# Kernel optimization log

Hardware: AMD Instinct MI355X
Metric: run time of the kernel (lower is better)

## Reference

```python
import jax, jax.numpy as jnp
import numpy as np

HIDDEN = 128
INPUT_DIM = 1
NUM_CLASSES = 2


def setup_inputs() -> dict:
    key = jax.random.key(0)
    ks = jax.random.split(key, 7)
    B, T = 256, 1024
    s_ih = 1.0 / np.sqrt(HIDDEN)
    x = jax.random.normal(ks[0], (B, T, INPUT_DIM), dtype=jnp.float32)
    W_ih = jax.random.uniform(ks[1], (HIDDEN, INPUT_DIM), jnp.float32, -s_ih, s_ih)
    W_hh = jax.random.uniform(ks[2], (HIDDEN, HIDDEN), jnp.float32, -s_ih, s_ih)
    b_ih = jax.random.uniform(ks[3], (HIDDEN,), jnp.float32, -s_ih, s_ih)
    b_hh = jax.random.uniform(ks[4], (HIDDEN,), jnp.float32, -s_ih, s_ih)
    W_fc = jax.random.uniform(ks[5], (NUM_CLASSES, HIDDEN), jnp.float32, -s_ih, s_ih)
    b_fc = jax.random.uniform(ks[6], (NUM_CLASSES,), jnp.float32, -s_ih, s_ih)
    return {"x": x, "W_ih": W_ih, "W_hh": W_hh, "b_ih": b_ih,
            "b_hh": b_hh, "W_fc": W_fc, "b_fc": b_fc}


def reference(x, W_ih, W_hh, b_ih, b_hh, W_fc, b_fc):
    B = x.shape[0]
    # Precompute input projection for all timesteps: [B,T,H]
    xp = jnp.einsum('bti,hi->bth', x, W_ih) + b_ih + b_hh
    h0 = jnp.zeros((B, HIDDEN), dtype=x.dtype)

    def step(h, xp_t):
        h_new = jnp.tanh(xp_t + h @ W_hh.T)  # [B,H]
        return h_new, h_new

    _, hs = jax.lax.scan(step, h0, jnp.swapaxes(xp, 0, 1))  # hs: [T,B,H]
    out = jnp.swapaxes(hs, 0, 1)  # [B,T,H]
    logits = jnp.einsum('bth,ch->btc', out, W_fc) + b_fc  # [B,T,C]
    return logits
```

## Files before the change

kernel.cpp:

```cpp
#include <hip/hip_runtime.h>

typedef float f32x2 __attribute__((ext_vector_type(2)));
typedef float f32x4 __attribute__((ext_vector_type(4)));

#define BB 256
#define TT 1024
#define HH 128
#define CC 2

__device__ __forceinline__ float ftanh(float u) {
    float e = __expf(2.0f * u);
    float r = __builtin_amdgcn_rcpf(e + 1.0f);
    return fmaf(-2.0f, r, 1.0f);
}

__device__ __forceinline__ float bcast(float v, int j) {
    return __int_as_float(__builtin_amdgcn_readlane(__float_as_int(v), j));
}

#define DPP_ADD(v, ctrl)                                                     \
    ((v) + __int_as_float(__builtin_amdgcn_mov_dpp(                          \
         __float_as_int(v), (ctrl), 0xF, 0xF, true)))

__device__ __forceinline__ float wave_sum(float q) {
    q = DPP_ADD(q, 0xB1);
    q = DPP_ADD(q, 0x4E);
    q = DPP_ADD(q, 0x124);
    q = DPP_ADD(q, 0x128);
    return bcast(q, 0) + bcast(q, 16) + bcast(q, 32) + bcast(q, 48);
}

__global__ __launch_bounds__(256, 1) void rnn_kernel(
    const float* __restrict__ x, const float* __restrict__ W_ih,
    const float* __restrict__ W_hh, const float* __restrict__ b_ih,
    const float* __restrict__ b_hh, const float* __restrict__ W_fc,
    const float* __restrict__ b_fc, float* __restrict__ out)
{
    const int b   = blockIdx.x;
    const int tid = threadIdx.x;
    const int l   = tid & 63;
    const int wv  = tid >> 6;
    const int lq  = l & 31;
    const int kb  = wv << 5;
    const int rA  = l, rB = l + 64;
    const int rF  = kb + lq;

    __shared__ float xs[TT + 8];
    __shared__ f32x2 p2[2][4][64];
    __shared__ f32x2 qp[4][4];

    {
        const f32x4* xr = (const f32x4*)(x + (size_t)b * TT);
        ((f32x4*)xs)[tid] = xr[tid];
    }
    if (tid < 8) xs[TT + tid] = 0.f;

    const float wih  = W_ih[rF];
    const float bias = b_ih[rF] + b_hh[rF];
    const float wf0  = 0.5f * W_fc[rF];
    const float wf1  = 0.5f * W_fc[HH + rF];
    const float bf0  = b_fc[0], bf1 = b_fc[1];

    float wa[32], wb[32];
    {
        const f32x4* a4 = (const f32x4*)(W_hh + (size_t)rA * HH + kb);
        const f32x4* b4 = (const f32x4*)(W_hh + (size_t)rB * HH + kb);
        #pragma unroll
        for (int j = 0; j < 8; ++j) {
            f32x4 va = a4[j], vb = b4[j];
            wa[4*j+0] = va.x; wa[4*j+1] = va.y; wa[4*j+2] = va.z; wa[4*j+3] = va.w;
            wb[4*j+0] = vb.x; wb[4*j+1] = vb.y; wb[4*j+2] = vb.z; wb[4*j+3] = vb.w;
        }
        #pragma unroll
        for (int k = 0; k < 32; ++k)
            asm volatile("" : "+v"(wa[k]), "+v"(wb[k]));
    }

    float hn = 0.f;
    float* o = out + (size_t)b * TT * CC;

    __syncthreads();
    float xcur = xs[0];

    #pragma unroll 4
    for (int t = 0; t < TT; ++t) {
        const int buf = t & 1, qb = t & 3;

        float aA0 = 0.f, aA1 = 0.f, aB0 = 0.f, aB1 = 0.f;
        #pragma unroll
        for (int k = 0; k < 32; k += 2) {
            float s0 = bcast(hn, k);
            float s1 = bcast(hn, k + 1);
            aA0 = fmaf(wa[k],     s0, aA0);
            aB0 = fmaf(wb[k],     s0, aB0);
            aA1 = fmaf(wa[k + 1], s1, aA1);
            aB1 = fmaf(wb[k + 1], s1, aB1);
        }
        f32x2 pr = { aA0 + aA1, aB0 + aB1 };
        p2[buf][wv][l] = pr;

        float q0 = wave_sum(wf0 * hn);
        float q1 = wave_sum(wf1 * hn);
        if (l == 0) qp[qb][wv] = f32x2{q0, q1};

        const float base  = fmaf(xcur, wih, bias);
        const float xnext = xs[t + 1];

        __syncthreads();

        if (t > 0 && tid == 0) {
            f32x2 s = (qp[qb][0] + qp[qb][1]) + (qp[qb][2] + qp[qb][3]);
            s.x += bf0; s.y += bf1;
            *(f32x2*)(o + (t - 1) * CC) = s;
        }

        const float* pf = (const float*)&p2[buf][0][0]
                        + ((((wv & 1) << 5) + lq) << 1) + (wv >> 1);
        float p0 = pf[0], p1 = pf[128], pv2 = pf[256], pv3 = pf[384];
        hn = ftanh(base + ((p0 + p1) + (pv2 + pv3)));
        xcur = xnext;
    }

    {
        float q0 = wave_sum(wf0 * hn);
        float q1 = wave_sum(wf1 * hn);
        if (l == 0) qp[0][wv] = f32x2{q0, q1};
    }
    __syncthreads();
    if (tid == 0) {
        f32x2 s = (qp[0][0] + qp[0][1]) + (qp[0][2] + qp[0][3]);
        s.x += bf0; s.y += bf1;
        *(f32x2*)(o + (TT - 1) * CC) = s;
    }
}

extern "C" void kernel_launch(void* const* d_in, const int* in_sizes, int n_in,
                              void* d_out, int out_size, void* d_ws, size_t ws_size,
                              hipStream_t stream) {
    const float* x    = (const float*)d_in[0];
    const float* W_ih = (const float*)d_in[1];
    const float* W_hh = (const float*)d_in[2];
    const float* b_ih = (const float*)d_in[3];
    const float* b_hh = (const float*)d_in[4];
    const float* W_fc = (const float*)d_in[5];
    const float* b_fc = (const float*)d_in[6];
    float* out = (float*)d_out;

    rnn_kernel<<<BB, 256, 0, stream>>>(x, W_ih, W_hh, b_ih, b_hh, W_fc, b_fc, out);
}
```

Measured before the change: 464.2 us.

## Process two batch rows per block with packed f32x2 FMAs

Each workgroup now advances two independent batch sequences at once, and the grid shrinks to half as many blocks. Weights are repacked as f32x2 pairs so the matvec can use packed FMA. The partial-sum LDS layout changes so each thread reads one f32x4 per row. The goal is to amortise the per-step barrier and latency over two recurrences and raise ILP, at the cost of only 128 blocks on a GPU with 256 CUs, which leaves many CUs idle.

Result: slower. 648.2 us (+39.6%).

```diff
diff --git a/kernel.cpp b/kernel.cpp
--- a/kernel.cpp
+++ b/kernel.cpp
@@ -7,6 +7,7 @@
 #define TT 1024
 #define HH 128
 #define CC 2
+#define NR 2
 
 __device__ __forceinline__ float ftanh(float u) {
     float e = __expf(2.0f * u);
@@ -45,15 +46,16 @@
     const int rA  = l, rB = l + 64;
     const int rF  = kb + lq;
 
-    __shared__ float xs[TT + 8];
-    __shared__ f32x2 p2[2][4][64];
-    __shared__ f32x2 qp[4][4];
+    __shared__ float xs[NR][TT + 8];
+    __shared__ float p2[2][NR][HH][4];
+    __shared__ f32x2 qp[4][NR][4];
 
-    {
-        const f32x4* xr = (const f32x4*)(x + (size_t)b * TT);
-        ((f32x4*)xs)[tid] = xr[tid];
+    #pragma unroll
+    for (int r = 0; r < NR; ++r) {
+        const f32x4* xr = (const f32x4*)(x + (size_t)(NR * b + r) * TT);
+        ((f32x4*)xs[r])[tid] = xr[tid];
     }
-    if (tid < 8) xs[TT + tid] = 0.f;
+    if (tid < 8) { xs[0][TT + tid] = 0.f; xs[1][TT + tid] = 0.f; }
 
     const float wih  = W_ih[rF];
     const float bias = b_ih[rF] + b_hh[rF];
@@ -61,76 +63,95 @@
     const float wf1  = 0.5f * W_fc[HH + rF];
     const float bf0  = b_fc[0], bf1 = b_fc[1];
 
-    float wa[32], wb[32];
+    f32x2 wr[32];
     {
         const f32x4* a4 = (const f32x4*)(W_hh + (size_t)rA * HH + kb);
         const f32x4* b4 = (const f32x4*)(W_hh + (size_t)rB * HH + kb);
         #pragma unroll
         for (int j = 0; j < 8; ++j) {
             f32x4 va = a4[j], vb = b4[j];
-            wa[4*j+0] = va.x; wa[4*j+1] = va.y; wa[4*j+2] = va.z; wa[4*j+3] = va.w;
-            wb[4*j+0] = vb.x; wb[4*j+1] = vb.y; wb[4*j+2] = vb.z; wb[4*j+3] = vb.w;
+            wr[4*j+0] = f32x2{va.x, vb.x};
+            wr[4*j+1] = f32x2{va.y, vb.y};
+            wr[4*j+2] = f32x2{va.z, vb.z};
+            wr[4*j+3] = f32x2{va.w, vb.w};
         }
-        #pragma unroll
-        for (int k = 0; k < 32; ++k)
-            asm volatile("" : "+v"(wa[k]), "+v"(wb[k]));
     }
 
-    float hn = 0.f;
-    float* o = out + (size_t)b * TT * CC;
+    float hn0 = 0.f, hn1 = 0.f;
+    float* oo = out + (size_t)(NR * b + (tid & 1)) * TT * CC;
 
     __syncthreads();
-    float xcur = xs[0];
+    float xc0 = xs[0][0], xc1 = xs[1][0];
 
     #pragma unroll 4
     for (int t = 0; t < TT; ++t) {
         const int buf = t & 1, qb = t & 3;
 
-        float aA0 = 0.f, aA1 = 0.f, aB0 = 0.f, aB1 = 0.f;
+        asm volatile("" : "+v"(wr[0]), "+v"(wr[1]), "+v"(wr[2]), "+v"(wr[3]),
+                          "+v"(wr[4]), "+v"(wr[5]), "+v"(wr[6]), "+v"(wr[7]));
+        asm volatile("" : "+v"(wr[8]), "+v"(wr[9]), "+v"(wr[10]), "+v"(wr[11]),
+                          "+v"(wr[12]), "+v"(wr[13]), "+v"(wr[14]), "+v"(wr[15]));
+        asm volatile("" : "+v"(wr[16]), "+v"(wr[17]), "+v"(wr[18]), "+v"(wr[19]),
+                          "+v"(wr[20]), "+v"(wr[21]), "+v"(wr[22]), "+v"(wr[23]));
+        asm volatile("" : "+v"(wr[24]), "+v"(wr[25]), "+v"(wr[26]), "+v"(wr[27]),
+                          "+v"(wr[28]), "+v"(wr[29]), "+v"(wr[30]), "+v"(wr[31]));
+
+        f32x2 a00 = {0.f,0.f}, a01 = {0.f,0.f};
+        f32x2 a10 = {0.f,0.f}, a11 = {0.f,0.f};
         #pragma unroll
         for (int k = 0; k < 32; k += 2) {
-            float s0 = bcast(hn, k);
-            float s1 = bcast(hn, k + 1);
-            aA0 = fmaf(wa[k],     s0, aA0);
-            aB0 = fmaf(wb[k],     s0, aB0);
-            aA1 = fmaf(wa[k + 1], s1, aA1);
-            aB1 = fmaf(wb[k + 1], s1, aB1);
+            float s00 = bcast(hn0, k), s01 = bcast(hn0, k + 1);
+            float s10 = bcast(hn1, k), s11 = bcast(hn1, k + 1);
+            a00 = __builtin_elementwise_fma(wr[k],     f32x2{s00, s00}, a00);
+            a10 = __builtin_elementwise_fma(wr[k],     f32x2{s10, s10}, a10);
+            a01 = __builtin_elementwise_fma(wr[k + 1], f32x2{s01, s01}, a01);
+            a11 = __builtin_elementwise_fma(wr[k + 1], f32x2{s11, s11}, a11);
         }
-        f32x2 pr = { aA0 + aA1, aB0 + aB1 };
-        p2[buf][wv][l] = pr;
+        f32x2 pr0 = a00 + a01, pr1 = a10 + a11;
 
-        float q0 = wave_sum(wf0 * hn);
-        float q1 = wave_sum(wf1 * hn);
-        if (l == 0) qp[qb][wv] = f32x2{q0, q1};
+        p2[buf][0][rA][wv] = pr0.x;  p2[buf][0][rB][wv] = pr0.y;
+        p2[buf][1][rA][wv] = pr1.x;  p2[buf][1][rB][wv] = pr1.y;
 
-        const float base  = fmaf(xcur, wih, bias);
-        const float xnext = xs[t + 1];
+        float q00 = wave_sum(wf0 * hn0), q01 = wave_sum(wf1 * hn0);
+        float q10 = wave_sum(wf0 * hn1), q11 = wave_sum(wf1 * hn1);
+        if (l == 0) {
+            qp[qb][0][wv] = f32x2{q00, q01};
+            qp[qb][1][wv] = f32x2{q10, q11};
+        }
+
+        const float base0 = fmaf(xc0, wih, bias);
+        const float base1 = fmaf(xc1, wih, bias);
+        xc0 = xs[0][t + 1];  xc1 = xs[1][t + 1];
 
         __syncthreads();
 
-        if (t > 0 && tid == 0) {
-            f32x2 s = (qp[qb][0] + qp[qb][1]) + (qp[qb][2] + qp[qb][3]);
+        if (t > 0 && tid < NR) {
+            f32x2 s = (qp[qb][tid][0] + qp[qb][tid][1])
+                    + (qp[qb][tid][2] + qp[qb][tid][3]);
             s.x += bf0; s.y += bf1;
-            *(f32x2*)(o + (t - 1) * CC) = s;
+            *(f32x2*)(oo + (t - 1) * CC) = s;
         }
 
-        const float* pf = (const float*)&p2[buf][0][0]
-                        + ((((wv & 1) << 5) + lq) << 1) + (wv >> 1);
-        float p0 = pf[0], p1 = pf[128], pv2 = pf[256], pv3 = pf[384];
-        hn = ftanh(base + ((p0 + p1) + (pv2 + pv3)));
-        xcur = xnext;
+        f32x4 c0 = *(const f32x4*)&p2[buf][0][rF][0];
+        f32x4 c1 = *(const f32x4*)&p2[buf][1][rF][0];
+        hn0 = ftanh(base0 + ((c0.x + c0.y) + (c0.z + c0.w)));
+        hn1 = ftanh(base1 + ((c1.x + c1.y) + (c1.z + c1.w)));
     }
 
     {
-        float q0 = wave_sum(wf0 * hn);
-        float q1 = wave_sum(wf1 * hn);
-        if (l == 0) qp[0][wv] = f32x2{q0, q1};
+        float q00 = wave_sum(wf0 * hn0), q01 = wave_sum(wf1 * hn0);
+        float q10 = wave_sum(wf0 * hn1), q11 = wave_sum(wf1 * hn1);
+        if (l == 0) {
+            qp[0][0][wv] = f32x2{q00, q01};
+            qp[0][1][wv] = f32x2{q10, q11};
+        }
     }
     __syncthreads();
-    if (tid == 0) {
-        f32x2 s = (qp[0][0] + qp[0][1]) + (qp[0][2] + qp[0][3]);
+    if (tid < NR) {
+        f32x2 s = (qp[0][tid][0] + qp[0][tid][1])
+                + (qp[0][tid][2] + qp[0][tid][3]);
         s.x += bf0; s.y += bf1;
-        *(f32x2*)(o + (TT - 1) * CC) = s;
+        *(f32x2*)(oo + (TT - 1) * CC) = s;
     }
 }
 
@@ -146,5 +167,5 @@
     const float* b_fc = (const float*)d_in[6];
     float* out = (float*)d_out;
 
-    rnn_kernel<<<BB, 256, 0, stream>>>(x, W_ih, W_hh, b_ih, b_hh, W_fc, b_fc, out);
+    rnn_kernel<<<BB / NR, 256, 0, stream>>>(x, W_ih, W_hh, b_ih, b_hh, W_fc, b_fc, out);
 }
```

## Pack two batch sequences per block and merge the FC lane reductions

Applied to the files above, without the earlier changes.

Each 512-thread block now runs two independent batch sequences, one per 256-thread group, so half as many blocks are launched and two recurrences share one CU and one barrier. The two output-class reductions are folded into one DPP reduction: the lower half-wave weights by class 0 and the upper half by class 1, which removes the 0.5 scaling and one full wave_sum per step. The empty asm register pin on the W_hh weights is dropped and launch bounds change to (512,2). The aim is to hide per-step latency by interleaving two recurrences on each SIMD. The risk is that the shared barrier couples the two groups and each CU now does twice the per-step work.

Measured after the change: 540.6 us. 16.5% more time.

```diff
diff --git a/kernel.cpp b/kernel.cpp
--- a/kernel.cpp
+++ b/kernel.cpp
@@ -7,6 +7,7 @@
 #define TT 1024
 #define HH 128
 #define CC 2
+#define NG 2
 
 __device__ __forceinline__ float ftanh(float u) {
     float e = __expf(2.0f * u);
@@ -22,15 +23,7 @@
     ((v) + __int_as_float(__builtin_amdgcn_mov_dpp(                          \
          __float_as_int(v), (ctrl), 0xF, 0xF, true)))
 
-__device__ __forceinline__ float wave_sum(float q) {
-    q = DPP_ADD(q, 0xB1);
-    q = DPP_ADD(q, 0x4E);
-    q = DPP_ADD(q, 0x124);
-    q = DPP_ADD(q, 0x128);
-    return bcast(q, 0) + bcast(q, 16) + bcast(q, 32) + bcast(q, 48);
-}
-
-__global__ __launch_bounds__(256, 1) void rnn_kernel(
+__global__ __launch_bounds__(512, 2) void rnn_kernel(
     const float* __restrict__ x, const float* __restrict__ W_ih,
     const float* __restrict__ W_hh, const float* __restrict__ b_ih,
     const float* __restrict__ b_hh, const float* __restrict__ W_fc,
@@ -38,27 +31,28 @@
 {
     const int b   = blockIdx.x;
     const int tid = threadIdx.x;
+    const int g   = tid >> 8;
+    const int t2  = tid & 255;
     const int l   = tid & 63;
-    const int wv  = tid >> 6;
+    const int wv  = (tid >> 6) & 3;
     const int lq  = l & 31;
     const int kb  = wv << 5;
     const int rA  = l, rB = l + 64;
     const int rF  = kb + lq;
 
-    __shared__ float xs[TT + 8];
-    __shared__ f32x2 p2[2][4][64];
-    __shared__ f32x2 qp[4][4];
+    __shared__ float xs[NG][TT + 8];
+    __shared__ f32x2 p2[2][NG][4][64];
+    __shared__ f32x2 qp[4][NG][4];
 
     {
-        const f32x4* xr = (const f32x4*)(x + (size_t)b * TT);
-        ((f32x4*)xs)[tid] = xr[tid];
+        const f32x4* xr = (const f32x4*)(x + (size_t)(NG * b + g) * TT);
+        ((f32x4*)xs[g])[t2] = xr[t2];
     }
-    if (tid < 8) xs[TT + tid] = 0.f;
+    if (t2 < 8) xs[g][TT + t2] = 0.f;
 
     const float wih  = W_ih[rF];
     const float bias = b_ih[rF] + b_hh[rF];
-    const float wf0  = 0.5f * W_fc[rF];
-    const float wf1  = 0.5f * W_fc[HH + rF];
+    const float wfs  = (l < 32) ? W_fc[rF] : W_fc[HH + rF];
     const float bf0  = b_fc[0], bf1 = b_fc[1];
 
     float wa[32], wb[32];
@@ -71,16 +65,13 @@
             wa[4*j+0] = va.x; wa[4*j+1] = va.y; wa[4*j+2] = va.z; wa[4*j+3] = va.w;
             wb[4*j+0] = vb.x; wb[4*j+1] = vb.y; wb[4*j+2] = vb.z; wb[4*j+3] = vb.w;
         }
-        #pragma unroll
-        for (int k = 0; k < 32; ++k)
-            asm volatile("" : "+v"(wa[k]), "+v"(wb[k]));
     }
 
     float hn = 0.f;
-    float* o = out + (size_t)b * TT * CC;
+    float* o = out + (size_t)(NG * b + g) * TT * CC;
 
     __syncthreads();
-    float xcur = xs[0];
+    float xcur = xs[g][0];
 
     #pragma unroll 4
     for (int t = 0; t < TT; ++t) {
@@ -97,24 +88,31 @@
             aB1 = fmaf(wb[k + 1], s1, aB1);
         }
         f32x2 pr = { aA0 + aA1, aB0 + aB1 };
-        p2[buf][wv][l] = pr;
+        p2[buf][g][wv][l] = pr;
 
-        float q0 = wave_sum(wf0 * hn);
-        float q1 = wave_sum(wf1 * hn);
-        if (l == 0) qp[qb][wv] = f32x2{q0, q1};
+        {
+            float q = wfs * hn;
+            q = DPP_ADD(q, 0xB1);
+            q = DPP_ADD(q, 0x4E);
+            q = DPP_ADD(q, 0x124);
+            q = DPP_ADD(q, 0x128);
+            float q0 = bcast(q, 0)  + bcast(q, 16);
+            float q1 = bcast(q, 32) + bcast(q, 48);
+            if (l == 0) qp[qb][g][wv] = f32x2{q0, q1};
+        }
 
         const float base  = fmaf(xcur, wih, bias);
-        const float xnext = xs[t + 1];
+        const float xnext = xs[g][t + 1];
 
         __syncthreads();
 
-        if (t > 0 && tid == 0) {
-            f32x2 s = (qp[qb][0] + qp[qb][1]) + (qp[qb][2] + qp[qb][3]);
+        if (t > 0 && t2 == 0) {
+            f32x2 s = (qp[qb][g][0] + qp[qb][g][1]) + (qp[qb][g][2] + qp[qb][g][3]);
             s.x += bf0; s.y += bf1;
             *(f32x2*)(o + (t - 1) * CC) = s;
         }
 
-        const float* pf = (const float*)&p2[buf][0][0]
+        const float* pf = (const float*)&p2[buf][g][0][0]
                         + ((((wv & 1) << 5) + lq) << 1) + (wv >> 1);
         float p0 = pf[0], p1 = pf[128], pv2 = pf[256], pv3 = pf[384];
         hn = ftanh(base + ((p0 + p1) + (pv2 + pv3)));
@@ -122,13 +120,18 @@
     }
 
     {
-        float q0 = wave_sum(wf0 * hn);
-        float q1 = wave_sum(wf1 * hn);
-        if (l == 0) qp[0][wv] = f32x2{q0, q1};
+        float q = wfs * hn;
+        q = DPP_ADD(q, 0xB1);
+        q = DPP_ADD(q, 0x4E);
+        q = DPP_ADD(q, 0x124);
+        q = DPP_ADD(q, 0x128);
+        float q0 = bcast(q, 0)  + bcast(q, 16);
+        float q1 = bcast(q, 32) + bcast(q, 48);
+        if (l == 0) qp[0][g][wv] = f32x2{q0, q1};
     }
     __syncthreads();
-    if (tid == 0) {
-        f32x2 s = (qp[0][0] + qp[0][1]) + (qp[0][2] + qp[0][3]);
+    if (t2 == 0) {
+        f32x2 s = (qp[0][g][0] + qp[0][g][1]) + (qp[0][g][2] + qp[0][g][3]);
         s.x += bf0; s.y += bf1;
         *(f32x2*)(o + (TT - 1) * CC) = s;
     }
@@ -146,5 +149,5 @@
     const float* b_fc = (const float*)d_in[6];
     float* out = (float*)d_out;
 
-    rnn_kernel<<<BB, 256, 0, stream>>>(x, W_ih, W_hh, b_ih, b_hh, W_fc, b_fc, out);
+    rnn_kernel<<<BB / NG, 512, 0, stream>>>(x, W_ih, W_hh, b_ih, b_hh, W_fc, b_fc, out);
 }
```

## Merge FC reductions, move output projection off critical path, batch logits stores

Applied to the files above, without the earlier changes.

The two per-class wave reductions become one. Each half-wave holds one class weight, and the result is split after the DPP steps. This reduction now runs after the barrier, alongside the p2 loads, and is consumed one step later, so it no longer sits between the matvec and the barrier. Logits go into a 16-entry shared ring and are written to global memory in 32-float bursts every 16 steps, replacing a small store each step. This adds extra step-lag bookkeeping and a tail flush that must exactly cover the last entries.

Measured after the change: 442.2 us. -4.7%, faster.

```diff
diff --git a/kernel.cpp b/kernel.cpp
--- a/kernel.cpp
+++ b/kernel.cpp
@@ -22,14 +22,6 @@
     ((v) + __int_as_float(__builtin_amdgcn_mov_dpp(                          \
          __float_as_int(v), (ctrl), 0xF, 0xF, true)))
 
-__device__ __forceinline__ float wave_sum(float q) {
-    q = DPP_ADD(q, 0xB1);
-    q = DPP_ADD(q, 0x4E);
-    q = DPP_ADD(q, 0x124);
-    q = DPP_ADD(q, 0x128);
-    return bcast(q, 0) + bcast(q, 16) + bcast(q, 32) + bcast(q, 48);
-}
-
 __global__ __launch_bounds__(256, 1) void rnn_kernel(
     const float* __restrict__ x, const float* __restrict__ W_ih,
     const float* __restrict__ W_hh, const float* __restrict__ b_ih,
@@ -48,6 +40,7 @@
     __shared__ float xs[TT + 8];
     __shared__ f32x2 p2[2][4][64];
     __shared__ f32x2 qp[4][4];
+    __shared__ f32x2 obuf[16];
 
     {
         const f32x4* xr = (const f32x4*)(x + (size_t)b * TT);
@@ -57,8 +50,7 @@
 
     const float wih  = W_ih[rF];
     const float bias = b_ih[rF] + b_hh[rF];
-    const float wf0  = 0.5f * W_fc[rF];
-    const float wf1  = 0.5f * W_fc[HH + rF];
+    const float wfs  = (l < 32) ? W_fc[rF] : W_fc[HH + rF];
     const float bf0  = b_fc[0], bf1 = b_fc[1];
 
     float wa[32], wb[32];
@@ -96,41 +88,61 @@
             aA1 = fmaf(wa[k + 1], s1, aA1);
             aB1 = fmaf(wb[k + 1], s1, aB1);
         }
-        f32x2 pr = { aA0 + aA1, aB0 + aB1 };
-        p2[buf][wv][l] = pr;
-
-        float q0 = wave_sum(wf0 * hn);
-        float q1 = wave_sum(wf1 * hn);
-        if (l == 0) qp[qb][wv] = f32x2{q0, q1};
-
-        const float base  = fmaf(xcur, wih, bias);
+        p2[buf][wv][l] = f32x2{ aA0 + aA1, aB0 + aB1 };
         const float xnext = xs[t + 1];
 
         __syncthreads();
 
-        if (t > 0 && tid == 0) {
-            f32x2 s = (qp[qb][0] + qp[qb][1]) + (qp[qb][2] + qp[qb][3]);
-            s.x += bf0; s.y += bf1;
-            *(f32x2*)(o + (t - 1) * CC) = s;
-        }
-
         const float* pf = (const float*)&p2[buf][0][0]
                         + ((((wv & 1) << 5) + lq) << 1) + (wv >> 1);
         float p0 = pf[0], p1 = pf[128], pv2 = pf[256], pv3 = pf[384];
+
+        {
+            float q = wfs * hn;
+            q = DPP_ADD(q, 0xB1);
+            q = DPP_ADD(q, 0x4E);
+            q = DPP_ADD(q, 0x124);
+            q = DPP_ADD(q, 0x128);
+            float q0 = bcast(q, 0)  + bcast(q, 16);
+            float q1 = bcast(q, 32) + bcast(q, 48);
+            if (l == 0) qp[qb][wv] = f32x2{q0, q1};
+        }
+        if (t >= 2 && tid == 0) {
+            const int pq = (t - 1) & 3;
+            f32x2 s = (qp[pq][0] + qp[pq][1]) + (qp[pq][2] + qp[pq][3]);
+            s.x += bf0; s.y += bf1;
+            obuf[(t - 2) & 15] = s;
+        }
+        if ((t & 15) == 1 && t >= 17 && tid < 32) {
+            ((float*)(o + (t - 17) * CC))[tid] = ((const float*)obuf)[tid];
+        }
+
+        const float base = fmaf(xcur, wih, bias);
+        xcur = xnext;
         hn = ftanh(base + ((p0 + p1) + (pv2 + pv3)));
-        xcur = xnext;
     }
 
     {
-        float q0 = wave_sum(wf0 * hn);
-        float q1 = wave_sum(wf1 * hn);
+        float q = wfs * hn;
+        q = DPP_ADD(q, 0xB1);
+        q = DPP_ADD(q, 0x4E);
+        q = DPP_ADD(q, 0x124);
+        q = DPP_ADD(q, 0x128);
+        float q0 = bcast(q, 0)  + bcast(q, 16);
+        float q1 = bcast(q, 32) + bcast(q, 48);
         if (l == 0) qp[0][wv] = f32x2{q0, q1};
     }
     __syncthreads();
     if (tid == 0) {
-        f32x2 s = (qp[0][0] + qp[0][1]) + (qp[0][2] + qp[0][3]);
+        f32x2 s = (qp[3][0] + qp[3][1]) + (qp[3][2] + qp[3][3]);
         s.x += bf0; s.y += bf1;
-        *(f32x2*)(o + (TT - 1) * CC) = s;
+        *(f32x2*)(o + (TT - 2) * CC) = s;
+        f32x2 s2 = (qp[0][0] + qp[0][1]) + (qp[0][2] + qp[0][3]);
+        s2.x += bf0; s2.y += bf1;
+        *(f32x2*)(o + (TT - 1) * CC) = s2;
+    }
+    if (tid < 28) {
+        ((float*)(o + 1008 * CC))[tid] = ((const float*)obuf)[tid];
     }
 }
 
```
